# Performance work log

Hardware: AMD Instinct MI355X
Metric: run time of the kernel (lower is better)

## Reference

```python
import jax, jax.numpy as jnp
import numpy as np

B, S, D, H, HD, MEM = 2, 2048, 1024, 16, 64, 512
SPARSITY_Q = 0.1


def setup_inputs() -> dict:
    key = jax.random.key(0)
    ks = jax.random.split(key, 12)
    s = 1.0 / np.sqrt(D).astype(np.float32)
    return {
        "hidden_states": jax.random.normal(ks[0], (B, S, D), jnp.float32),
        "attention_mask": jnp.ones((B, S), jnp.int32),
        "past_k": jax.random.normal(ks[1], (B, H, MEM, HD), jnp.float32),
        "past_v": jax.random.normal(ks[2], (B, H, MEM, HD), jnp.float32),
        "Wq": jax.random.normal(ks[3], (D, D), jnp.float32) * s,
        "bq": jnp.zeros((D,), jnp.float32),
        "Wk": jax.random.normal(ks[4], (D, D), jnp.float32) * s,
        "bk": jnp.zeros((D,), jnp.float32),
        "Wv": jax.random.normal(ks[5], (D, D), jnp.float32) * s,
        "bv": jnp.zeros((D,), jnp.float32),
        "Wo": jax.random.normal(ks[6], (D, D), jnp.float32) * s,
        "bo": jnp.zeros((D,), jnp.float32),
    }


def reference(hidden_states, attention_mask, past_k, past_v,
              Wq, bq, Wk, bk, Wv, bv, Wo, bo):
    b, s, d = hidden_states.shape
    # projections -> [b, h, s, hd]
    def split_heads(x):
        return x.reshape(b, s, H, HD).transpose(0, 2, 1, 3)
    q = split_heads(hidden_states @ Wq + bq)
    k = split_heads(hidden_states @ Wk + bk)
    v = split_heads(hidden_states @ Wv + bv)
    # concat KV cache along key length
    k = jnp.concatenate([past_k, k], axis=2)  # [b, h, mem+s, hd]
    v = jnp.concatenate([past_v, v], axis=2)
    past_len = past_k.shape[2]
    mask = jnp.concatenate(
        [jnp.ones((b, past_len), attention_mask.dtype), attention_mask], axis=1)
    scale = 1.0 / float(np.sqrt(HD))
    scores = jnp.einsum("bhqd,bhkd->bhqk", q, k) * scale  # [b,h,s,mem+s]
    # per-row quantile threshold sparsification (torch.quantile, linear interp)
    thr = jnp.quantile(scores, SPARSITY_Q, axis=-1, keepdims=True)
    neg_inf = jnp.float32(-jnp.inf)
    scores = jnp.where(scores < thr, neg_inf, scores)
    scores = jnp.where(mask[:, None, None, :] == 0, neg_inf, scores)
    attn = jax.nn.softmax(scores, axis=-1)  # dropout is identity in eval
    out = jnp.einsum("bhqk,bhkd->bhqd", attn, v)
    out = out.transpose(0, 2, 1, 3).reshape(b, s, d) @ Wo + bo
    new_k = k[:, :, -MEM:, :]
    new_v = v[:, :, -MEM:, :]
    return out, (new_k, new_v)
```

## Files before the change

### kernel.cpp

```cpp
#include <hip/hip_runtime.h>
#include <stdint.h>

typedef unsigned short ushort_t;
typedef __attribute__((ext_vector_type(8))) short bf16x8;
typedef __attribute__((ext_vector_type(4))) float f32x4;

#define BB 2
#define SS 2048
#define DD 1024
#define HH 16
#define HDD 64
#define MEMM 512
#define KTOT 2560
#define NKB 80
#define NTILE 160


__device__ __forceinline__ float bf2f(uint32_t u) {
    return __uint_as_float(u << 16);
}
__device__ __forceinline__ ushort_t f2bf(float f) {
    uint32_t u = __float_as_uint(f);
    uint32_t r = (u + 0x7FFFu + ((u >> 16) & 1u)) >> 16;
    return (ushort_t)r;
}
__device__ __forceinline__ uint32_t mapkey(uint32_t u) {
    return (u & 0x8000u) ? (0xFFFFu ^ u) : (u | 0x8000u);
}
__device__ __forceinline__ uint32_t unmapkey(uint32_t k) {
    return (k & 0x8000u) ? (k ^ 0x8000u) : (0xFFFFu ^ k);
}

__global__ __launch_bounds__(256) void cast_hidden_kernel(
    const float* __restrict__ h, ushort_t* __restrict__ hb)
{
    size_t i0 = ((size_t)blockIdx.x * 256 + threadIdx.x) * 16;
    ushort_t o[16];
#pragma unroll
    for (int j = 0; j < 4; ++j) {
        float4 v = *(const float4*)&h[i0 + j * 4];
        o[j * 4 + 0] = f2bf(v.x); o[j * 4 + 1] = f2bf(v.y);
        o[j * 4 + 2] = f2bf(v.z); o[j * 4 + 3] = f2bf(v.w);
    }
    *(uint4*)&hb[i0] = *(uint4*)&o[0];
    *(uint4*)&hb[i0 + 8] = *(uint4*)&o[8];
}

__global__ __launch_bounds__(256) void transw_kernel(
    const float* __restrict__ Wq, const float* __restrict__ Wk,
    const float* __restrict__ Wv, const float* __restrict__ Wo,
    ushort_t* __restrict__ WtAll)
{
    __shared__ ushort_t T[64][66];
    const int z = blockIdx.z;
    const float* W = (z == 0) ? Wq : (z == 1) ? Wk : (z == 2) ? Wv : Wo;
    ushort_t* dst = WtAll + (size_t)z * DD * DD;
    const int k0 = blockIdx.x * 64, n0 = blockIdx.y * 64;
    const int t = threadIdx.x;
    const int kk = t >> 2, c4 = (t & 3) * 16;
#pragma unroll
    for (int j = 0; j < 4; ++j) {
        float4 v = *(const float4*)&W[(size_t)(k0 + kk) * DD + n0 + c4 + j * 4];
        T[kk][c4 + j * 4 + 0] = f2bf(v.x);
        T[kk][c4 + j * 4 + 1] = f2bf(v.y);
        T[kk][c4 + j * 4 + 2] = f2bf(v.z);
        T[kk][c4 + j * 4 + 3] = f2bf(v.w);
    }
    __syncthreads();
    const int nn = t >> 2, kc = (t & 3) * 16;
    ushort_t tmp[16];
#pragma unroll
    for (int j = 0; j < 16; ++j) tmp[j] = T[kc + j][nn];
    *(uint4*)&dst[(size_t)(n0 + nn) * DD + k0 + kc] = *(uint4*)&tmp[0];
    *(uint4*)&dst[(size_t)(n0 + nn) * DD + k0 + kc + 8] = *(uint4*)&tmp[8];
}

__global__ __launch_bounds__(256) void gemm128_kernel(
    const ushort_t* __restrict__ A, const ushort_t* __restrict__ Bt, int mode,
    const float* __restrict__ bq, const float* __restrict__ bk, const float* __restrict__ bv,
    float* __restrict__ outf,
    ushort_t* __restrict__ q_bf, ushort_t* __restrict__ kbf, ushort_t* __restrict__ vbf,
    float* __restrict__ nk, float* __restrict__ nv)
{
    __shared__ __align__(16) ushort_t As[128 * 32];
    __shared__ __align__(16) ushort_t Bs[128 * 32];
    const int tid = threadIdx.x;
    const int lane = tid & 63, w = tid >> 6;
    const int wm = w >> 1, wn = w & 1;
    const int row16 = lane & 15, quad = lane >> 4;
    const int n0 = blockIdx.x * 128, m0 = blockIdx.y * 128;

    const int r0 = tid >> 2, c0 = (tid & 3) * 8;
    const int r1 = (tid + 256) >> 2, c1 = ((tid + 256) & 3) * 8;

    f32x4 acc[4][4];
#pragma unroll
    for (int i = 0; i < 4; ++i)
#pragma unroll
        for (int j = 0; j < 4; ++j) acc[i][j] = (f32x4){0.f, 0.f, 0.f, 0.f};

    for (int k0 = 0; k0 < DD; k0 += 32) {
        *(uint4*)&As[tid * 8]         = *(const uint4*)&A [(size_t)(m0 + r0) * DD + k0 + c0];
        *(uint4*)&As[(tid + 256) * 8] = *(const uint4*)&A [(size_t)(m0 + r1) * DD + k0 + c1];
        *(uint4*)&Bs[tid * 8]         = *(const uint4*)&Bt[(size_t)(n0 + r0) * DD + k0 + c0];
        *(uint4*)&Bs[(tid + 256) * 8] = *(const uint4*)&Bt[(size_t)(n0 + r1) * DD + k0 + c1];
        __syncthreads();
        bf16x8 af[4], bfr[4];
#pragma unroll
        for (int mt = 0; mt < 4; ++mt)
            af[mt] = *(const bf16x8*)&As[(wm * 64 + mt * 16 + row16) * 32 + quad * 8];
#pragma unroll
        for (int nt = 0; nt < 4; ++nt)
            bfr[nt] = *(const bf16x8*)&Bs[(wn * 64 + nt * 16 + row16) * 32 + quad * 8];
#pragma unroll
        for (int mt = 0; mt < 4; ++mt)
#pragma unroll
            for (int nt = 0; nt < 4; ++nt)
                acc[mt][nt] = __builtin_amdgcn_mfma_f32_16x16x32_bf16(
                    af[mt], bfr[nt], acc[mt][nt], 0, 0, 0);
        __syncthreads();
    }

#pragma unroll
    for (int nt = 0; nt < 4; ++nt) {
        const int nb = n0 + wn * 64 + nt * 16;
        if (mode == 0) {
#pragma unroll
            for (int mt = 0; mt < 4; ++mt) {
#pragma unroll
                for (int r = 0; r < 4; ++r) {
                    int m = m0 + wm * 64 + mt * 16 + quad * 4 + r;
                    int n = nb + row16;
                    outf[(size_t)m * DD + n] = acc[mt][nt][r] + bq[n];
                }
            }
        } else {
            const int sel = nb >> 10;
            const float* bias = (sel == 0) ? bq : (sel == 1) ? bk : bv;
#pragma unroll
            for (int mt = 0; mt < 4; ++mt) {
#pragma unroll
                for (int r = 0; r < 4; ++r) {
                    int m = m0 + wm * 64 + mt * 16 + quad * 4 + r;
                    int nn = (nb + row16) & 1023;
                    float v = acc[mt][nt][r] + bias[nn];
                    int b = m >> 11, s = m & (SS - 1);
                    int h = nn >> 6, d = nn & 63;
                    size_t bh = (size_t)b * HH + h;
                    if (sel == 0) {
                        q_bf[(bh * SS + s) * HDD + d] = f2bf(v);
                    } else {
                        ushort_t* dst = (sel == 1) ? kbf : vbf;
                        dst[(bh * KTOT + MEMM + s) * HDD + d] = f2bf(v);
                        if (s >= SS - MEMM) {
                            float* nf = (sel == 1) ? nk : nv;
                            nf[(bh * MEMM + (s - (SS - MEMM))) * HDD + d] = v;
                        }
                    }
                }
            }
        }
    }
}

__global__ __launch_bounds__(256) void cast_past_kernel(
    const float* __restrict__ pk, const float* __restrict__ pv,
    ushort_t* __restrict__ kbf, ushort_t* __restrict__ vbf)
{
    int idx = blockIdx.x * 256 + threadIdx.x;
    int bh = idx >> 15;
    int rem = idx & 32767;
    size_t dst = (size_t)bh * KTOT * HDD + rem;
    kbf[dst] = f2bf(pk[idx]);
    vbf[dst] = f2bf(pv[idx]);
}

__global__ __launch_bounds__(256) void transpose_v_kernel(
    const ushort_t* __restrict__ vbf, ushort_t* __restrict__ vt)
{
    __shared__ ushort_t T[64][72];
    const int k0 = blockIdx.x * 64;
    const int bh = blockIdx.y;
    const int t = threadIdx.x;
    const int rr = t >> 3, cc = (t & 7) * 8;
#pragma unroll
    for (int p = 0; p < 2; ++p) {
        int kk = p * 32 + rr;
        *(uint4*)&T[kk][cc] =
            *(const uint4*)(vbf + ((size_t)bh * KTOT + k0 + kk) * HDD + cc);
    }
    __syncthreads();
    const int ld = t & 63, nt = t >> 6;
    const int sr = ld & 15, q = ld >> 4;
#pragma unroll
    for (int kbl = 0; kbl < 2; ++kbl) {
        ushort_t tmp[8];
#pragma unroll
        for (int j = 0; j < 8; ++j) tmp[j] = T[kbl * 32 + q * 8 + j][nt * 16 + sr];
        *(uint4*)(vt + (((size_t)bh * NKB + (k0 >> 5) + kbl) * 4 + nt) * 512 + ld * 8)
            = *(uint4*)tmp;
    }
}

__device__ __forceinline__ uint32_t wave_iscan(uint32_t x, int lane) {
#pragma unroll
    for (int d = 1; d < 64; d <<= 1) {
        uint32_t t = __shfl_up(x, d, 64);
        if (lane >= d) x += t;
    }
    return x;
}
__device__ __forceinline__ void select_from_counts(
    const uint32_t* c, uint32_t R, int lane, uint32_t* bin_out, uint32_t* rem_out)
{
    uint32_t s = c[0] + c[1] + c[2] + c[3];
    uint32_t incl = wave_iscan(s, lane);
    uint32_t excl = incl - s;
    uint64_t bal = __ballot(incl > R);
    int fl = __ffsll((unsigned long long)bal) - 1;
    uint32_t exf = __shfl(excl, fl, 64);
    uint32_t c0 = __shfl(c[0], fl, 64), c1 = __shfl(c[1], fl, 64);
    uint32_t c2 = __shfl(c[2], fl, 64), c3 = __shfl(c[3], fl, 64);
    uint32_t cc[4] = {c0, c1, c2, c3};
    uint32_t cum = exf, bin = fl * 4, rem = 0;
#pragma unroll
    for (int i = 0; i < 4; ++i) {
        if (cum + cc[i] > R) { bin = fl * 4 + i; rem = R - cum; break; }
        cum += cc[i];
    }
    *bin_out = bin;
    *rem_out = rem;
}

__device__ __forceinline__ uint32_t select768(
    const uint32_t* Hr, uint32_t T, int lane)
{
    uint32_t wd[6];
    uint32_t s = 0;
#pragma unroll
    for (int i = 0; i < 6; ++i) {
        wd[i] = Hr[lane * 6 + i];
        s += (wd[i] & 0xFFFFu) + (wd[i] >> 16);
    }
    uint32_t incl = wave_iscan(s, lane);
    uint32_t excl = incl - s;
    uint64_t bal = __ballot(incl > T);
    int fl = __ffsll((unsigned long long)bal) - 1;
    uint32_t cum = __shfl(excl, fl, 64);
    uint32_t wf[6];
#pragma unroll
    for (int i = 0; i < 6; ++i) wf[i] = __shfl(wd[i], fl, 64);
    uint32_t o = (uint32_t)fl * 12u;
#pragma unroll
    for (int i = 0; i < 12; ++i) {
        uint32_t cnt = (wf[i >> 1] >> ((i & 1) * 16)) & 0xFFFFu;
        if (cum + cnt > T) { o = (uint32_t)fl * 12u + (uint32_t)i; break; }
        cum += cnt;
    }
    return o;
}

__global__ __launch_bounds__(1024) void fused_attn_kernel(
    const ushort_t* __restrict__ qbf, const ushort_t* __restrict__ kbf,
    const ushort_t* __restrict__ vt, const int* __restrict__ amask,
    ushort_t* __restrict__ attn_bf)
{
    __shared__ __align__(16) ushort_t S[NTILE * 256];
    __shared__ uint32_t H[16][385];
    __shared__ uint32_t cw[16][16];
    __shared__ float thrs[16];
    __shared__ uint32_t fb[2];

    const int tid = threadIdx.x;
    const int w = tid >> 6, lane = tid & 63;
    const int row16 = lane & 15, quad = lane >> 4;
    const int bid = blockIdx.x;
    const int xcd = bid & 7, slot = bid >> 3;
    const int bh = xcd * 4 + (slot >> 7);
    const int pnl = slot & 127;
    const int b = bh >> 4, h = bh & 15;
    const int m0 = pnl * 16;
    uint32_t* Hf = &H[0][0];

    for (int i = tid; i < 16 * 385; i += 1024) Hf[i] = 0u;
    __syncthreads();

    const ushort_t* qrow = qbf + ((size_t)bh * SS + m0 + row16) * HDD + quad * 8;
    bf16x8 q0 = *(const bf16x8*)qrow;
    bf16x8 q1 = *(const bf16x8*)(qrow + 32);
    const ushort_t* kbase = kbf + ((size_t)bh * KTOT + w * 160 + row16) * HDD + quad * 8;

    uint4 rka[2], rkb[2];
    rka[0] = *(const uint4*)(kbase);
    rkb[0] = *(const uint4*)(kbase + 32);
    rka[1] = *(const uint4*)(kbase + (size_t)16 * HDD);
    rkb[1] = *(const uint4*)(kbase + (size_t)16 * HDD + 32);

    uint32_t nBel = 0, nReg = 0;
    for (int i = 0; i < 10; ++i) {
        bf16x8 af0, af1;
        *(uint4*)&af0 = rka[i & 1];
        *(uint4*)&af1 = rkb[i & 1];
        if (i + 2 < 10) {
            rka[i & 1] = *(const uint4*)(kbase + (size_t)(i + 2) * 16 * HDD);
            rkb[i & 1] = *(const uint4*)(kbase + (size_t)(i + 2) * 16 * HDD + 32);
        }
        f32x4 acc = {0.f, 0.f, 0.f, 0.f};
        acc = __builtin_amdgcn_mfma_f32_16x16x32_bf16(af0, q0, acc, 0, 0, 0);
        acc = __builtin_amdgcn_mfma_f32_16x16x32_bf16(af1, q1, acc, 0, 0, 0);
        uint32_t p0, p1;
        float s0 = acc[0] * 0.125f, s1 = acc[1] * 0.125f;
        float s2 = acc[2] * 0.125f, s3 = acc[3] * 0.125f;
        asm("v_cvt_pk_bf16_f32 %0, %1, %2" : "=v"(p0) : "v"(s0), "v"(s1));
        asm("v_cvt_pk_bf16_f32 %0, %1, %2" : "=v"(p1) : "v"(s2), "v"(s3));
        uint2 pp; pp.x = p0; pp.y = p1;
        *(uint2*)&S[(w * 10 + i) * 256 + lane * 4] = pp;
        uint32_t ww2[2] = {p0, p1};
#pragma unroll
        for (int q = 0; q < 2; ++q) {
            uint32_t t0 = (ww2[q] >> 8) & 255u, lo0 = ww2[q] & 255u;
            uint32_t t1 = ww2[q] >> 24,         lo1 = (ww2[q] >> 16) & 255u;
            nBel += (t0 >= 0xC1u);
            nBel += (t1 >= 0xC1u);
            uint32_t cls0 = 0xC0u - t0;
            uint32_t cls1 = 0xC0u - t1;
            if (cls0 <= 2u) {
                ++nReg;
                uint32_t o = cls0 * 256u + (lo0 ^ 255u);
                atomicAdd(&H[row16][o >> 1], 1u << ((o & 1u) << 4));
            }
            if (cls1 <= 2u) {
                ++nReg;
                uint32_t o = cls1 * 256u + (lo1 ^ 255u);
                atomicAdd(&H[row16][o >> 1], 1u << ((o & 1u) << 4));
            }
        }
    }
    uint32_t pk2 = nBel | (nReg << 16);
    pk2 += (uint32_t)__shfl_xor(pk2, 16, 64);
    pk2 += (uint32_t)__shfl_xor(pk2, 32, 64);
    if (lane < 16) cw[w][lane] = pk2;
    __syncthreads();

    {
        uint32_t P = 0;
#pragma unroll
        for (int ww = 0; ww < 16; ++ww) P += cw[ww][w];
        const uint32_t c0v = P & 0xFFFFu;
        const uint32_t c3v = c0v + (P >> 16);
        if (c0v <= 255u && c3v > 256u) {
            uint32_t o0 = select768(&H[w][0], 255u - c0v, lane);
            uint32_t o1 = select768(&H[w][0], 256u - c0v, lane);
            uint32_t rawA = ((0xC0u - (o0 >> 8)) << 8) | ((o0 & 255u) ^ 255u);
            uint32_t rawB = ((0xC0u - (o1 >> 8)) << 8) | ((o1 & 255u) ^ 255u);
            if (lane == 0)
                thrs[w] = bf2f(rawA) + 0.9f * (bf2f(rawB) - bf2f(rawA));
        }
    }

    bool okl = false;
    if (lane < 16) {
        uint32_t Pl = 0;
#pragma unroll
        for (int ww = 0; ww < 16; ++ww) Pl += cw[ww][lane];
        uint32_t c0l = Pl & 0xFFFFu, c3l = c0l + (Pl >> 16);
        okl = (c0l <= 255u) && (c3l > 256u);
    }
    uint32_t fail = (uint32_t)__ballot(lane < 16 && !okl) & 0xFFFFu;
    while (fail) {
        const int rho = __ffs(fail) - 1; fail &= fail - 1;
        uint32_t rawAB[2] = {0u, 0u};
#pragma unroll
        for (int t2 = 0; t2 < 2; ++t2) {
            __syncthreads();
            for (int i = tid; i < 257; i += 1024) Hf[i] = 0u;
            __syncthreads();
            for (int k = tid; k < KTOT; k += 1024) {
                uint32_t val = S[(k >> 4) * 256 + (((k & 15) >> 2) * 16 + rho) * 4 + (k & 3)];
                atomicAdd(&Hf[mapkey(val) >> 8], 1u);
            }
            __syncthreads();
            if (w == 0) {
                uint32_t c4[4];
#pragma unroll
                for (int i = 0; i < 4; ++i) c4[i] = Hf[lane * 4 + i];
                uint32_t binM, rem;
                select_from_counts(c4, 255u + (uint32_t)t2, lane, &binM, &rem);
                if (lane == 0) { fb[0] = binM; fb[1] = rem; }
            }
            __syncthreads();
            const uint32_t binM = fb[0], rem = fb[1];
            for (int i = tid; i < 257; i += 1024) Hf[i] = 0u;
            __syncthreads();
            for (int k = tid; k < KTOT; k += 1024) {
                uint32_t val = S[(k >> 4) * 256 + (((k & 15) >> 2) * 16 + rho) * 4 + (k & 3)];
                uint32_t mk = mapkey(val);
                if ((mk >> 8) == binM) atomicAdd(&Hf[mk & 255u], 1u);
            }
            __syncthreads();
            if (w == 0) {
                uint32_t c4[4];
#pragma unroll
                for (int i = 0; i < 4; ++i) c4[i] = Hf[lane * 4 + i];
                uint32_t low, r2;
                select_from_counts(c4, rem, lane, &low, &r2);
                rawAB[t2] = unmapkey((binM << 8) | low);
            }
        }
        __syncthreads();
        if (tid == 0) {
            float fA = bf2f(rawAB[0]), fB = bf2f(rawAB[1]);
            thrs[rho] = fA + 0.9f * (fB - fA);
        }
        __syncthreads();
    }
    __syncthreads();

    const float thr = thrs[row16];
    const int* amq = amask + b * SS + quad * 8;
    const ushort_t* bbase = vt + (size_t)bh * NKB * 2048 + lane * 8;

    const uint32_t ow = (row16 == 0) ? 0x3F803F80u : 0u;
    uint4 ov; ov.x = ow; ov.y = ow; ov.z = ow; ov.w = ow;
    bf16x8 onesf; *(uint4*)&onesf = ov;

    f32x4 acc[4];
#pragma unroll
    for (int i = 0; i < 4; ++i) acc[i] = (f32x4){0.f, 0.f, 0.f, 0.f};
    f32x4 acc5 = (f32x4){0.f, 0.f, 0.f, 0.f};

    const int kb0 = w * 5, kbe = kb0 + 5;
    const int sA = ((quad & 1) * 32 + row16) * 4;
    const int sB = sA + 64;

    uint4 b_nxt[4];
#pragma unroll
    for (int nt = 0; nt < 4; ++nt)
        b_nxt[nt] = *(const uint4*)(bbase + (size_t)kb0 * 2048 + nt * 512);
    int4 m_nxt0 = {1, 1, 1, 1}, m_nxt1 = {1, 1, 1, 1};
    if (kb0 * 32 >= MEMM) {
        m_nxt0 = *(const int4*)(amq + kb0 * 32 - MEMM);
        m_nxt1 = *(const int4*)(amq + kb0 * 32 - MEMM + 4);
    }

    for (int kb = kb0; kb < kbe; ++kb) {
        uint4 b_cur[4] = {b_nxt[0], b_nxt[1], b_nxt[2], b_nxt[3]};
        int4 mc0 = m_nxt0, mc1 = m_nxt1;
        const int kbn = kb + 1;
        if (kbn < kbe) {
#pragma unroll
            for (int nt = 0; nt < 4; ++nt)
                b_nxt[nt] = *(const uint4*)(bbase + (size_t)kbn * 2048 + nt * 512);
            const int kn = kbn * 32;
            if (kn >= MEMM) {
                m_nxt0 = *(const int4*)(amq + kn - MEMM);
                m_nxt1 = *(const int4*)(amq + kn - MEMM + 4);
            }
        }
        const int tS = (2 * kb + (quad >> 1)) * 256;
        uint2 g0 = *(const uint2*)&S[tS + sA];
        uint2 g1 = *(const uint2*)&S[tS + sB];
        uint32_t u[8] = {g0.x & 0xFFFFu, g0.x >> 16, g0.y & 0xFFFFu, g0.y >> 16,
                         g1.x & 0xFFFFu, g1.x >> 16, g1.y & 0xFFFFu, g1.y >> 16};
        int mm[8] = {mc0.x, mc0.y, mc0.z, mc0.w, mc1.x, mc1.y, mc1.z, mc1.w};
        const bool masked = (kb * 32 >= MEMM);
        float wv[8];
#pragma unroll
        for (int j = 0; j < 8; ++j) {
            float s = bf2f(u[j]);
            bool keep = (s >= thr);
            if (masked) keep = keep && (mm[j] != 0);
            wv[j] = keep ? __expf(s) : 0.f;
        }
        uint4 aq;
        asm("v_cvt_pk_bf16_f32 %0, %1, %2" : "=v"(aq.x) : "v"(wv[0]), "v"(wv[1]));
        asm("v_cvt_pk_bf16_f32 %0, %1, %2" : "=v"(aq.y) : "v"(wv[2]), "v"(wv[3]));
        asm("v_cvt_pk_bf16_f32 %0, %1, %2" : "=v"(aq.z) : "v"(wv[4]), "v"(wv[5]));
        asm("v_cvt_pk_bf16_f32 %0, %1, %2" : "=v"(aq.w) : "v"(wv[6]), "v"(wv[7]));
        bf16x8 af;
        *(uint4*)&af = aq;
#pragma unroll
        for (int nt = 0; nt < 4; ++nt) {
            bf16x8 bf;
            *(uint4*)&bf = b_cur[nt];
            acc[nt] = __builtin_amdgcn_mfma_f32_16x16x32_bf16(af, bf, acc[nt], 0, 0, 0);
        }
        acc5 = __builtin_amdgcn_mfma_f32_16x16x32_bf16(af, onesf, acc5, 0, 0, 0);
    }

    __syncthreads();
    float* redf = (float*)S;
#define RED(i) (redf + ((size_t)(i) * 64 + lane) * 21)
    if (w >= 8) {
        float* d = RED(w - 8);
#pragma unroll
        for (int nt = 0; nt < 4; ++nt)
#pragma unroll
            for (int r = 0; r < 4; ++r) d[nt * 4 + r] = acc[nt][r];
#pragma unroll
        for (int r = 0; r < 4; ++r) d[16 + r] = acc5[r];
    }
    __syncthreads();
    if (w < 8) {
        const float* s = RED(w);
#pragma unroll
        for (int nt = 0; nt < 4; ++nt)
#pragma unroll
            for (int r = 0; r < 4; ++r) acc[nt][r] += s[nt * 4 + r];
#pragma unroll
        for (int r = 0; r < 4; ++r) acc5[r] += s[16 + r];
    }
    __syncthreads();
    if (w >= 4 && w < 8) {
        float* d = RED(w - 4);
#pragma unroll
        for (int nt = 0; nt < 4; ++nt)
#pragma unroll
            for (int r = 0; r < 4; ++r) d[nt * 4 + r] = acc[nt][r];
#pragma unroll
        for (int r = 0; r < 4; ++r) d[16 + r] = acc5[r];
    }
    __syncthreads();
    if (w < 4) {
        const float* s = RED(w);
#pragma unroll
        for (int nt = 0; nt < 4; ++nt)
#pragma unroll
            for (int r = 0; r < 4; ++r) acc[nt][r] += s[nt * 4 + r];
#pragma unroll
        for (int r = 0; r < 4; ++r) acc5[r] += s[16 + r];
    }
    __syncthreads();
    if (w >= 2 && w < 4) {
        float* d = RED(w - 2);
#pragma unroll
        for (int nt = 0; nt < 4; ++nt)
#pragma unroll
            for (int r = 0; r < 4; ++r) d[nt * 4 + r] = acc[nt][r];
#pragma unroll
        for (int r = 0; r < 4; ++r) d[16 + r] = acc5[r];
    }
    __syncthreads();
    if (w < 2) {
        const float* s = RED(w);
#pragma unroll
        for (int nt = 0; nt < 4; ++nt)
#pragma unroll
            for (int r = 0; r < 4; ++r) acc[nt][r] += s[nt * 4 + r];
#pragma unroll
        for (int r = 0; r < 4; ++r) acc5[r] += s[16 + r];
    }
    __syncthreads();
    if (w == 1) {
        float* d = RED(0);
#pragma unroll
        for (int nt = 0; nt < 4; ++nt)
#pragma unroll
            for (int r = 0; r < 4; ++r) d[nt * 4 + r] = acc[nt][r];
#pragma unroll
        for (int r = 0; r < 4; ++r) d[16 + r] = acc5[r];
    }
    __syncthreads();
    if (w == 0) {
        const float* s = RED(0);
#pragma unroll
        for (int nt = 0; nt < 4; ++nt)
#pragma unroll
            for (int r = 0; r < 4; ++r) acc[nt][r] += s[nt * 4 + r];
#pragma unroll
        for (int r = 0; r < 4; ++r) acc5[r] += s[16 + r];

        float rinv[4];
#pragma unroll
        for (int r = 0; r < 4; ++r) {
            float rs = __shfl(acc5[r], quad * 16, 64);
            rinv[r] = 1.0f / rs;
        }
#pragma unroll
        for (int nt = 0; nt < 4; ++nt) {
#pragma unroll
            for (int r = 0; r < 4; ++r) {
                int row = quad * 4 + r;
                float val = acc[nt][r] * rinv[r];
                attn_bf[((size_t)b * SS + m0 + row) * DD + h * HDD + nt * 16 + row16] = f2bf(val);
            }
        }
    }
#undef RED
}

extern "C" void kernel_launch(void* const* d_in, const int* in_sizes, int n_in,
                              void* d_out, int out_size, void* d_ws, size_t ws_size,
                              hipStream_t stream)
{
    const float* hidden = (const float*)d_in[0];
    const int*   amask  = (const int*)d_in[1];
    const float* past_k = (const float*)d_in[2];
    const float* past_v = (const float*)d_in[3];
    const float* Wq = (const float*)d_in[4];
    const float* bq = (const float*)d_in[5];
    const float* Wk = (const float*)d_in[6];
    const float* bk = (const float*)d_in[7];
    const float* Wv = (const float*)d_in[8];
    const float* bv = (const float*)d_in[9];
    const float* Wo = (const float*)d_in[10];
    const float* bo = (const float*)d_in[11];

    float* out    = (float*)d_out;
    float* nk_out = out + (size_t)BB * SS * DD;
    float* nv_out = nk_out + (size_t)BB * HH * MEMM * HDD;

    char* base = (char*)d_ws;
    size_t off = 0;
    auto alloc = [&](size_t bytes) {
        char* p = base + off;
        off += (bytes + 255) & ~(size_t)255;
        return p;
    };
    ushort_t* hb    = (ushort_t*)alloc((size_t)BB * SS * DD * 2);
    ushort_t* WtAll = (ushort_t*)alloc((size_t)4 * DD * DD * 2);
    ushort_t* q_bf  = (ushort_t*)alloc((size_t)BB * HH * SS * HDD * 2);
    ushort_t* kbf   = (ushort_t*)alloc((size_t)BB * HH * KTOT * HDD * 2);
    ushort_t* vbf   = (ushort_t*)alloc((size_t)BB * HH * KTOT * HDD * 2);
    ushort_t* vt    = (ushort_t*)alloc((size_t)BB * HH * NKB * 4 * 512 * 2);
    ushort_t* abf   = (ushort_t*)alloc((size_t)BB * SS * DD * 2);

    dim3 blk(256);

    cast_hidden_kernel<<<dim3(1024), blk, 0, stream>>>(hidden, hb);
    transw_kernel<<<dim3(16, 16, 4), blk, 0, stream>>>(Wq, Wk, Wv, Wo, WtAll);
    gemm128_kernel<<<dim3(24, 32), blk, 0, stream>>>(
        hb, WtAll, 1, bq, bk, bv, nullptr, q_bf, kbf, vbf, nk_out, nv_out);
    cast_past_kernel<<<dim3(4096), blk, 0, stream>>>(past_k, past_v, kbf, vbf);
    transpose_v_kernel<<<dim3(KTOT / 64, BB * HH), blk, 0, stream>>>(vbf, vt);

    fused_attn_kernel<<<dim3(BB * HH * (SS / 16)), dim3(1024), 0, stream>>>(
        q_bf, kbf, vt, amask, abf);

    gemm128_kernel<<<dim3(8, 32), blk, 0, stream>>>(
        abf, WtAll + (size_t)3 * DD * DD, 0, bo, nullptr, nullptr, out,
        nullptr, nullptr, nullptr, nullptr, nullptr);
}
```

Measured before the change: 536.7 us.

## Keep attention scores in registers instead of LDS score tile

Score fragments from the QK MFMA are kept in per-lane registers rather than written to a shared-memory score tile. To make this work, the V-transpose kernel permutes the key order within each 32-key block so the score register layout lines up directly with the PV MFMA A-operand, and the mask loads are reindexed to match. The fallback exact-quantile histogram now reads scores from the owning lanes' registers. This removes the large LDS score buffer, which frees shared memory for occupancy and drops LDS stores and loads. In exchange it adds register pressure from ten held fragments, and the manual K and V prefetch pipelining is replaced by fully unrolled loops.

```diff
diff --git a/kernel.cpp b/kernel.cpp
--- a/kernel.cpp
+++ b/kernel.cpp
@@ -196,7 +196,8 @@
     for (int kbl = 0; kbl < 2; ++kbl) {
         ushort_t tmp[8];
 #pragma unroll
-        for (int j = 0; j < 8; ++j) tmp[j] = T[kbl * 32 + q * 8 + j][nt * 16 + sr];
+        for (int j = 0; j < 8; ++j)
+            tmp[j] = T[kbl * 32 + (j >> 2) * 16 + q * 4 + (j & 3)][nt * 16 + sr];
         *(uint4*)(vt + (((size_t)bh * NKB + (k0 >> 5) + kbl) * 4 + nt) * 512 + ld * 8)
             = *(uint4*)tmp;
     }
@@ -265,8 +266,7 @@
     const ushort_t* __restrict__ vt, const int* __restrict__ amask,
     ushort_t* __restrict__ attn_bf)
 {
-    __shared__ __align__(16) ushort_t S[NTILE * 256];
-    __shared__ uint32_t H[16][385];
+    __shared__ __align__(16) uint32_t U[8 * 64 * 21];
     __shared__ uint32_t cw[16][16];
     __shared__ float thrs[16];
     __shared__ uint32_t fb[2];
@@ -280,9 +280,10 @@
     const int pnl = slot & 127;
     const int b = bh >> 4, h = bh & 15;
     const int m0 = pnl * 16;
-    uint32_t* Hf = &H[0][0];
-
-    for (int i = tid; i < 16 * 385; i += 1024) Hf[i] = 0u;
+    uint32_t (*H)[385] = (uint32_t(*)[385])U;
+    uint32_t* Hf = U;
+
+    for (int i = tid; i < 16 * 385; i += 1024) U[i] = 0u;
     __syncthreads();
 
     const ushort_t* qrow = qbf + ((size_t)bh * SS + m0 + row16) * HDD + quad * 8;
@@ -290,31 +291,21 @@
     bf16x8 q1 = *(const bf16x8*)(qrow + 32);
     const ushort_t* kbase = kbf + ((size_t)bh * KTOT + w * 160 + row16) * HDD + quad * 8;
 
-    uint4 rka[2], rkb[2];
-    rka[0] = *(const uint4*)(kbase);
-    rkb[0] = *(const uint4*)(kbase + 32);
-    rka[1] = *(const uint4*)(kbase + (size_t)16 * HDD);
-    rkb[1] = *(const uint4*)(kbase + (size_t)16 * HDD + 32);
-
+    uint2 sc[10];
     uint32_t nBel = 0, nReg = 0;
+#pragma unroll
     for (int i = 0; i < 10; ++i) {
-        bf16x8 af0, af1;
-        *(uint4*)&af0 = rka[i & 1];
-        *(uint4*)&af1 = rkb[i & 1];
-        if (i + 2 < 10) {
-            rka[i & 1] = *(const uint4*)(kbase + (size_t)(i + 2) * 16 * HDD);
-            rkb[i & 1] = *(const uint4*)(kbase + (size_t)(i + 2) * 16 * HDD + 32);
-        }
-        f32x4 acc = {0.f, 0.f, 0.f, 0.f};
-        acc = __builtin_amdgcn_mfma_f32_16x16x32_bf16(af0, q0, acc, 0, 0, 0);
-        acc = __builtin_amdgcn_mfma_f32_16x16x32_bf16(af1, q1, acc, 0, 0, 0);
+        bf16x8 af0 = *(const bf16x8*)(kbase + (size_t)i * 16 * HDD);
+        bf16x8 af1 = *(const bf16x8*)(kbase + (size_t)i * 16 * HDD + 32);
+        f32x4 a4 = {0.f, 0.f, 0.f, 0.f};
+        a4 = __builtin_amdgcn_mfma_f32_16x16x32_bf16(af0, q0, a4, 0, 0, 0);
+        a4 = __builtin_amdgcn_mfma_f32_16x16x32_bf16(af1, q1, a4, 0, 0, 0);
         uint32_t p0, p1;
-        float s0 = acc[0] * 0.125f, s1 = acc[1] * 0.125f;
-        float s2 = acc[2] * 0.125f, s3 = acc[3] * 0.125f;
+        float s0 = a4[0] * 0.125f, s1 = a4[1] * 0.125f;
+        float s2 = a4[2] * 0.125f, s3 = a4[3] * 0.125f;
         asm("v_cvt_pk_bf16_f32 %0, %1, %2" : "=v"(p0) : "v"(s0), "v"(s1));
         asm("v_cvt_pk_bf16_f32 %0, %1, %2" : "=v"(p1) : "v"(s2), "v"(s3));
-        uint2 pp; pp.x = p0; pp.y = p1;
-        *(uint2*)&S[(w * 10 + i) * 256 + lane * 4] = pp;
+        sc[i].x = p0; sc[i].y = p1;
         uint32_t ww2[2] = {p0, p1};
 #pragma unroll
         for (int q = 0; q < 2; ++q) {
@@ -375,9 +366,15 @@
             __syncthreads();
             for (int i = tid; i < 257; i += 1024) Hf[i] = 0u;
             __syncthreads();
-            for (int k = tid; k < KTOT; k += 1024) {
-                uint32_t val = S[(k >> 4) * 256 + (((k & 15) >> 2) * 16 + rho) * 4 + (k & 3)];
-                atomicAdd(&Hf[mapkey(val) >> 8], 1u);
+            if (row16 == rho) {
+#pragma unroll
+                for (int i = 0; i < 10; ++i) {
+                    uint32_t xx = sc[i].x, yy = sc[i].y;
+                    atomicAdd(&Hf[mapkey(xx & 0xFFFFu) >> 8], 1u);
+                    atomicAdd(&Hf[mapkey(xx >> 16) >> 8], 1u);
+                    atomicAdd(&Hf[mapkey(yy & 0xFFFFu) >> 8], 1u);
+                    atomicAdd(&Hf[mapkey(yy >> 16) >> 8], 1u);
+                }
             }
             __syncthreads();
             if (w == 0) {
@@ -392,10 +389,17 @@
             const uint32_t binM = fb[0], rem = fb[1];
             for (int i = tid; i < 257; i += 1024) Hf[i] = 0u;
             __syncthreads();
-            for (int k = tid; k < KTOT; k += 1024) {
-                uint32_t val = S[(k >> 4) * 256 + (((k & 15) >> 2) * 16 + rho) * 4 + (k & 3)];
-                uint32_t mk = mapkey(val);
-                if ((mk >> 8) == binM) atomicAdd(&Hf[mk & 255u], 1u);
+            if (row16 == rho) {
+#pragma unroll
+                for (int i = 0; i < 10; ++i) {
+                    uint32_t kk4[4] = {sc[i].x & 0xFFFFu, sc[i].x >> 16,
+                                       sc[i].y & 0xFFFFu, sc[i].y >> 16};
+#pragma unroll
+                    for (int q = 0; q < 4; ++q) {
+                        uint32_t mk = mapkey(kk4[q]);
+                        if ((mk >> 8) == binM) atomicAdd(&Hf[mk & 255u], 1u);
+                    }
+                }
             }
             __syncthreads();
             if (w == 0) {
@@ -417,7 +421,7 @@
     __syncthreads();
 
     const float thr = thrs[row16];
-    const int* amq = amask + b * SS + quad * 8;
+    const int* amq2 = amask + b * SS + quad * 4;
     const ushort_t* bbase = vt + (size_t)bh * NKB * 2048 + lane * 8;
 
     const uint32_t ow = (row16 == 0) ? 0x3F803F80u : 0u;
@@ -429,48 +433,30 @@
     for (int i = 0; i < 4; ++i) acc[i] = (f32x4){0.f, 0.f, 0.f, 0.f};
     f32x4 acc5 = (f32x4){0.f, 0.f, 0.f, 0.f};
 
-    const int kb0 = w * 5, kbe = kb0 + 5;
-    const int sA = ((quad & 1) * 32 + row16) * 4;
-    const int sB = sA + 64;
-
-    uint4 b_nxt[4];
-#pragma unroll
-    for (int nt = 0; nt < 4; ++nt)
-        b_nxt[nt] = *(const uint4*)(bbase + (size_t)kb0 * 2048 + nt * 512);
-    int4 m_nxt0 = {1, 1, 1, 1}, m_nxt1 = {1, 1, 1, 1};
-    if (kb0 * 32 >= MEMM) {
-        m_nxt0 = *(const int4*)(amq + kb0 * 32 - MEMM);
-        m_nxt1 = *(const int4*)(amq + kb0 * 32 - MEMM + 4);
-    }
-
-    for (int kb = kb0; kb < kbe; ++kb) {
-        uint4 b_cur[4] = {b_nxt[0], b_nxt[1], b_nxt[2], b_nxt[3]};
-        int4 mc0 = m_nxt0, mc1 = m_nxt1;
-        const int kbn = kb + 1;
-        if (kbn < kbe) {
-#pragma unroll
-            for (int nt = 0; nt < 4; ++nt)
-                b_nxt[nt] = *(const uint4*)(bbase + (size_t)kbn * 2048 + nt * 512);
-            const int kn = kbn * 32;
-            if (kn >= MEMM) {
-                m_nxt0 = *(const int4*)(amq + kn - MEMM);
-                m_nxt1 = *(const int4*)(amq + kn - MEMM + 4);
-            }
-        }
-        const int tS = (2 * kb + (quad >> 1)) * 256;
-        uint2 g0 = *(const uint2*)&S[tS + sA];
-        uint2 g1 = *(const uint2*)&S[tS + sB];
-        uint32_t u[8] = {g0.x & 0xFFFFu, g0.x >> 16, g0.y & 0xFFFFu, g0.y >> 16,
-                         g1.x & 0xFFFFu, g1.x >> 16, g1.y & 0xFFFFu, g1.y >> 16};
-        int mm[8] = {mc0.x, mc0.y, mc0.z, mc0.w, mc1.x, mc1.y, mc1.z, mc1.w};
-        const bool masked = (kb * 32 >= MEMM);
+#pragma unroll
+    for (int j = 0; j < 5; ++j) {
+        const int kb = w * 5 + j;
+        uint4 bfrag[4];
+#pragma unroll
+        for (int nt = 0; nt < 4; ++nt)
+            bfrag[nt] = *(const uint4*)(bbase + (size_t)kb * 2048 + nt * 512);
+        const bool masked = (kb >= 16);
+        int4 mv0 = {1, 1, 1, 1}, mv1 = {1, 1, 1, 1};
+        if (masked) {
+            mv0 = *(const int4*)(amq2 + kb * 32 - MEMM);
+            mv1 = *(const int4*)(amq2 + kb * 32 - MEMM + 16);
+        }
+        const uint2 sA = sc[2 * j], sB = sc[2 * j + 1];
+        uint32_t u[8] = {sA.x & 0xFFFFu, sA.x >> 16, sA.y & 0xFFFFu, sA.y >> 16,
+                         sB.x & 0xFFFFu, sB.x >> 16, sB.y & 0xFFFFu, sB.y >> 16};
+        int mm[8] = {mv0.x, mv0.y, mv0.z, mv0.w, mv1.x, mv1.y, mv1.z, mv1.w};
         float wv[8];
 #pragma unroll
-        for (int j = 0; j < 8; ++j) {
-            float s = bf2f(u[j]);
+        for (int e = 0; e < 8; ++e) {
+            float s = bf2f(u[e]);
             bool keep = (s >= thr);
-            if (masked) keep = keep && (mm[j] != 0);
-            wv[j] = keep ? __expf(s) : 0.f;
+            if (masked) keep = keep && (mm[e] != 0);
+            wv[e] = keep ? __expf(s) : 0.f;
         }
         uint4 aq;
         asm("v_cvt_pk_bf16_f32 %0, %1, %2" : "=v"(aq.x) : "v"(wv[0]), "v"(wv[1]));
@@ -482,14 +468,14 @@
 #pragma unroll
         for (int nt = 0; nt < 4; ++nt) {
             bf16x8 bf;
-            *(uint4*)&bf = b_cur[nt];
+            *(uint4*)&bf = bfrag[nt];
             acc[nt] = __builtin_amdgcn_mfma_f32_16x16x32_bf16(af, bf, acc[nt], 0, 0, 0);
         }
         acc5 = __builtin_amdgcn_mfma_f32_16x16x32_bf16(af, onesf, acc5, 0, 0, 0);
     }
 
     __syncthreads();
-    float* redf = (float*)S;
+    float* redf = (float*)U;
 #define RED(i) (redf + ((size_t)(i) * 64 + lane) * 21)
     if (w >= 8) {
         float* d = RED(w - 8);
```

Result: faster. 509.7 us (-5.0%).
